# Performance work log

Hardware: AMD Instinct MI355X
Metric: run time of the kernel (lower is better)

## Reference

```python
import jax, jax.numpy as jnp
import numpy as np

EPS = 1e-5

def conv1x1(x, w, b):
    # x: (B,C,H,W), w: (O,C), b: (O,)
    return jnp.einsum('bchw,oc->bohw', x, w) + b[None, :, None, None]

def instance_norm(x):
    mu = jnp.mean(x, axis=(2, 3), keepdims=True)
    var = jnp.var(x, axis=(2, 3), keepdims=True)
    return (x - mu) / jnp.sqrt(var + EPS)

def setup_inputs() -> dict:
    key = jax.random.key(0)
    C = 256
    ks = jax.random.split(key, 16)
    def w(k):
        return jax.random.normal(k, (C, C), dtype=jnp.float32) * 0.02
    def b(k):
        return jax.random.normal(k, (C,), dtype=jnp.float32) * 0.01
    return {
        'x': jax.random.normal(ks[0], (8, C, 128, 128), dtype=jnp.float32),
        'wq1': w(ks[1]), 'bq1': b(ks[2]), 'wq2': w(ks[3]), 'bq2': b(ks[4]),
        'wk1': w(ks[5]), 'bk1': b(ks[6]), 'wk2': w(ks[7]), 'bk2': b(ks[8]),
        'wv': w(ks[9]), 'bv': b(ks[10]),
        'wg': w(ks[11]), 'bg': b(ks[12]),
        'wo': w(ks[13]), 'bo': b(ks[14]),
    }

def reference(x, wq1, bq1, wq2, bq2, wk1, bk1, wk2, bk2, wv, bv, wg, bg, wo, bo):
    head = 4
    B, C, H, W = x.shape
    c = C // head  # per-head channels
    n = H * W
    x = instance_norm(x)
    q = jax.nn.softplus(conv1x1(jax.nn.gelu(conv1x1(x, wq1, bq1), approximate=False), wq2, bq2))
    k = jax.nn.softplus(conv1x1(jax.nn.gelu(conv1x1(x, wk1, bk1), approximate=False), wk2, bk2))
    v = jax.nn.gelu(conv1x1(x, wv, bv), approximate=False)
    g = jax.nn.gelu(conv1x1(x, wg, bg), approximate=False)
    # b (head c) h w -> b head c (h w)
    q = q.reshape(B, head, c, n)
    kk = k.reshape(B, head, c, n)
    vv = v.reshape(B, head, c, n)
    kv = jnp.einsum('bhcn,bhdn->bhcd', kk, vv)  # (B,head,c,c)
    scale = 1.0 / jnp.sqrt(jnp.float32(c))
    z = jnp.einsum('bhcn,bhc->bhn', q, kk.sum(axis=-1)) * scale
    z = 1.0 / (z + jnp.float32(n))
    out = jnp.einsum('bhcn,bhcd->bhdn', q, kv) * scale
    out = (out + vv) * z[:, :, None, :]
    out = out.reshape(B, C, H, W)
    out = out * g
    return conv1x1(out, wo, bo)
```

## Files before the change

### kernel.cpp

```cpp
#include <hip/hip_runtime.h>
#include <stdint.h>

typedef short bf8 __attribute__((ext_vector_type(8)));
typedef short s4v __attribute__((ext_vector_type(4)));
typedef float f32x4 __attribute__((ext_vector_type(4)));

__device__ __forceinline__ short f2bf(float f){
  union { float f; unsigned u; } c; c.f = f;
  unsigned r = (c.u + 0x7fffu + ((c.u >> 16) & 1u)) >> 16;
  return (short)r;
}
__device__ __forceinline__ float bf2f(short s){
  union { unsigned u; float f; } c; c.u = ((unsigned)(unsigned short)s) << 16;
  return c.f;
}
__device__ __forceinline__ void gload16(const void* g, void* l){
  __builtin_amdgcn_global_load_lds((const __attribute__((address_space(1))) uint32_t*)g,
                                   (__attribute__((address_space(3))) uint32_t*)l, 16, 0, 0);
}
__device__ __forceinline__ float fast_erf(float x){
  const float s = fabsf(x);
  const float t = __builtin_amdgcn_rcpf(fmaf(0.3275911f, s, 1.0f));
  float p = fmaf(1.061405429f, t, -1.453152027f);
  p = fmaf(p, t, 1.421413741f);
  p = fmaf(p, t, -0.284496736f);
  p = fmaf(p, t, 0.254829592f);
  p = p * t;
  const float e = __expf(-s * s);
  return copysignf(fmaf(-p, e, 1.0f), x);
}
__device__ __forceinline__ float act_gelu(float x){
  return 0.5f * x * (1.0f + fast_erf(x * 0.70710678118654752f));
}
__device__ __forceinline__ float act_softplus(float x){
  const float e = __expf(-fabsf(x));
  return fmaxf(x, 0.0f) + __logf(1.0f + e);
}

__global__ __launch_bounds__(256) void k_statst(const float* __restrict__ x, short* __restrict__ xt,
                                                float* __restrict__ ps1, float* __restrict__ ps2){
  const int n0 = blockIdx.x * 64, c0 = blockIdx.y * 64, b = blockIdx.z;
  __shared__ short lt[64][68];
  const int t = threadIdx.x, nj = (t & 15) * 4, cb = t >> 4;
  float s1[4] = {0.f,0.f,0.f,0.f}, s2[4] = {0.f,0.f,0.f,0.f};
#pragma unroll
  for (int it = 0; it < 4; ++it){
    const int ci = cb + it * 16;
    const int row = b * 256 + c0 + ci;
    float4 v = *(const float4*)(x + (size_t)row * 16384 + n0 + nj);
    s4v o;
    o[0] = f2bf(v.x); o[1] = f2bf(v.y); o[2] = f2bf(v.z); o[3] = f2bf(v.w);
    *(s4v*)(&lt[ci][nj]) = o;
    s1[it] += v.x + v.y + v.z + v.w;
    s2[it] += v.x*v.x + v.y*v.y + v.z*v.z + v.w*v.w;
  }
  __syncthreads();
#pragma unroll
  for (int p = 0; p < 2; ++p){
    const int q = p * 256 + t;
    const int nl = q >> 3, c8 = (q & 7) * 8;
    bf8 o;
#pragma unroll
    for (int j = 0; j < 8; ++j) o[j] = lt[c8 + j][nl];
    *(bf8*)(xt + ((size_t)(b * 16384 + n0 + nl)) * 256 + c0 + c8) = o;
  }
#pragma unroll
  for (int it = 0; it < 4; ++it){
#pragma unroll
    for (int off = 8; off > 0; off >>= 1){
      s1[it] += __shfl_down(s1[it], off);
      s2[it] += __shfl_down(s2[it], off);
    }
  }
  if ((t & 15) == 0){
#pragma unroll
    for (int it = 0; it < 4; ++it){
      const int c = c0 + cb + it * 16;
      ps1[((size_t)(b * 256 + c)) * 256 + blockIdx.x] = s1[it];
      ps2[((size_t)(b * 256 + c)) * 256 + blockIdx.x] = s2[it];
    }
  }
}

__global__ __launch_bounds__(256) void k_red(const float* __restrict__ ps1, const float* __restrict__ ps2,
                                             float* __restrict__ mu, float* __restrict__ rsig){
  const int bc = blockIdx.x;
  const int t = threadIdx.x;
  __shared__ float a1[256], a2[256];
  a1[t] = ps1[(size_t)bc * 256 + t];
  a2[t] = ps2[(size_t)bc * 256 + t];
  __syncthreads();
  for (int s = 128; s > 0; s >>= 1){
    if (t < s){ a1[t] += a1[t+s]; a2[t] += a2[t+s]; }
    __syncthreads();
  }
  if (t == 0){
    float m = a1[0] * (1.0f/16384.0f);
    float v = a2[0] * (1.0f/16384.0f) - m*m;
    mu[bc] = m; rsig[bc] = rsqrtf(v + 1e-5f);
  }
}

__global__ __launch_bounds__(256) void k_norm(short* xn, const float* __restrict__ mu,
                                              const float* __restrict__ rsig){
  const int g = blockIdx.x * 256 + threadIdx.x;
#pragma unroll
  for (int pass = 0; pass < 8; ++pass){
    const int idx = g + pass * 524288;
    const int bn = idx >> 5, c8 = idx & 31;
    const int b = bn >> 14;
    const float* mp = mu + b * 256 + c8 * 8;
    const float* rp = rsig + b * 256 + c8 * 8;
    float4 m0 = *(const float4*)mp, m1 = *(const float4*)(mp + 4);
    float4 r0 = *(const float4*)rp, r1 = *(const float4*)(rp + 4);
    float mm[8] = {m0.x,m0.y,m0.z,m0.w,m1.x,m1.y,m1.z,m1.w};
    float rr[8] = {r0.x,r0.y,r0.z,r0.w,r1.x,r1.y,r1.z,r1.w};
    bf8 v = *(const bf8*)(xn + (size_t)idx * 8);
    bf8 o;
#pragma unroll
    for (int j = 0; j < 8; ++j) o[j] = f2bf((bf2f(v[j]) - mm[j]) * rr[j]);
    *(bf8*)(xn + (size_t)idx * 8) = o;
  }
}

__global__ __launch_bounds__(256) void k_wconv(const float* w0, const float* w1, const float* w2,
                                               const float* w3, const float* w4, const float* w5,
                                               const float* w6, short* __restrict__ wb){
  const int gid = blockIdx.x * 256 + threadIdx.x;
  const int mat = gid >> 14, r4 = gid & 16383;
  const float* srcs[7] = {w0, w1, w2, w3, w4, w5, w6};
  float4 v = *(const float4*)(srcs[mat] + (size_t)r4 * 4);
  s4v o; o[0] = f2bf(v.x); o[1] = f2bf(v.y); o[2] = f2bf(v.z); o[3] = f2bf(v.w);
  *(s4v*)(wb + (size_t)mat * 65536 + r4 * 4) = o;
}

template<int ACT>
__global__ __launch_bounds__(256, 2)
void k_gemm0(const short* __restrict__ A, const short* __restrict__ W,
             const float* __restrict__ bias, short* __restrict__ outp){
  __shared__ short sA[2][128 * 32];
  __shared__ short sB[2][256 * 32];
  const int t = threadIdx.x, l = t & 63, w = t >> 6;
  const int wr = w >> 1, wc = w & 1;
  const int lm = l & 15, lk = l >> 4;
  const size_t m0 = (size_t)blockIdx.x * 128;
  const int swz = ((lk ^ ((lm >> 1) & 3)) << 4);
  f32x4 acc[4][8] = {};

  auto stage = [&](int ks, int buf){
    const int k0 = ks * 32;
#pragma unroll
    for (int p = 0; p < 2; ++p){
      const int q = p * 256 + t, r = q >> 2, kc = q & 3;
      gload16(A + (m0 + r) * 256 + k0 + ((kc ^ ((r >> 1) & 3)) << 3),
              (char*)(&sA[buf][0]) + (p * 256 + w * 64) * 16);
    }
#pragma unroll
    for (int p = 0; p < 4; ++p){
      const int q = p * 256 + t, r = q >> 2, kc = q & 3;
      gload16(W + (size_t)r * 256 + k0 + ((kc ^ ((r >> 1) & 3)) << 3),
              (char*)(&sB[buf][0]) + (p * 256 + w * 64) * 16);
    }
  };

  stage(0, 0);
  __syncthreads();
  int cur = 0;
  for (int ks = 0; ks < 8; ++ks){
    if (ks < 7) stage(ks + 1, cur ^ 1);
    bf8 af[4], bfv[8];
#pragma unroll
    for (int mi = 0; mi < 4; ++mi)
      af[mi] = *(const bf8*)((const char*)(&sA[cur][0]) + (wr * 64 + mi * 16 + lm) * 64 + swz);
#pragma unroll
    for (int ni = 0; ni < 8; ++ni)
      bfv[ni] = *(const bf8*)((const char*)(&sB[cur][0]) + (wc * 128 + ni * 16 + lm) * 64 + swz);
#pragma unroll
    for (int mi = 0; mi < 4; ++mi)
#pragma unroll
      for (int ni = 0; ni < 8; ++ni)
        acc[mi][ni] = __builtin_amdgcn_mfma_f32_16x16x32_bf16(bfv[ni], af[mi], acc[mi][ni], 0, 0, 0);
    __syncthreads();
    cur ^= 1;
  }

#pragma unroll
  for (int ni = 0; ni < 8; ++ni){
    const int ob = wc * 128 + ni * 16 + lk * 4;
    const float4 b4 = *(const float4*)(bias + ob);
#pragma unroll
    for (int mi = 0; mi < 4; ++mi){
      const int px = wr * 64 + mi * 16 + lm;
      s4v o4;
#pragma unroll
      for (int j = 0; j < 4; ++j){
        float v = acc[mi][ni][j] + ((const float*)&b4)[j];
        if (ACT == 1) v = act_gelu(v);
        else if (ACT == 2) v = act_softplus(v);
        o4[j] = f2bf(v);
      }
      *(s4v*)(outp + (m0 + px) * 256 + ob) = o4;
    }
  }
}

__global__ __launch_bounds__(256, 2)
void k_chain(const short* __restrict__ A, const short* __restrict__ W1, const float* __restrict__ b1,
             const short* __restrict__ W2, const float* __restrict__ b2, short* __restrict__ out){
  __shared__ short sA[2][64 * 32];
  __shared__ short sB[2][256 * 32];
  __shared__ short h1[64 * 256];
  const int t = threadIdx.x, l = t & 63, w = t >> 6;
  const int lm = l & 15, lk = l >> 4;
  const size_t m0 = (size_t)blockIdx.x * 64;
  const int swz = ((lk ^ ((lm >> 1) & 3)) << 4);
  f32x4 acc[4][4] = {};

  auto stageA = [&](int ks, int buf){
    const int r = t >> 2, kc = t & 3;
    gload16(A + (m0 + r) * 256 + ks * 32 + ((kc ^ ((r >> 1) & 3)) << 3),
            (char*)(&sA[buf][0]) + w * 1024);
  };
  auto stageW = [&](const short* Wm, int ks, int buf){
#pragma unroll
    for (int p = 0; p < 4; ++p){
      const int q = p * 256 + t, r = q >> 2, kc = q & 3;
      gload16(Wm + (size_t)r * 256 + ks * 32 + ((kc ^ ((r >> 1) & 3)) << 3),
              (char*)(&sB[buf][0]) + (p * 256 + w * 64) * 16);
    }
  };

  stageA(0, 0); stageW(W1, 0, 0);
  __syncthreads();
  int cur = 0;
  for (int ks = 0; ks < 8; ++ks){
    if (ks < 7){ stageA(ks + 1, cur ^ 1); stageW(W1, ks + 1, cur ^ 1); }
    bf8 af[4], bfv[4];
#pragma unroll
    for (int mi = 0; mi < 4; ++mi)
      af[mi] = *(const bf8*)((const char*)(&sA[cur][0]) + (mi * 16 + lm) * 64 + swz);
#pragma unroll
    for (int ni = 0; ni < 4; ++ni)
      bfv[ni] = *(const bf8*)((const char*)(&sB[cur][0]) + (w * 64 + ni * 16 + lm) * 64 + swz);
#pragma unroll
    for (int mi = 0; mi < 4; ++mi)
#pragma unroll
      for (int ni = 0; ni < 4; ++ni)
        acc[mi][ni] = __builtin_amdgcn_mfma_f32_16x16x32_bf16(bfv[ni], af[mi], acc[mi][ni], 0, 0, 0);
    __syncthreads();
    cur ^= 1;
  }

  stageW(W2, 0, 0);
#pragma unroll
  for (int ni = 0; ni < 4; ++ni){
    const int ob = w * 64 + ni * 16 + lk * 4;
    const float4 b4 = *(const float4*)(b1 + ob);
#pragma unroll
    for (int mi = 0; mi < 4; ++mi){
      const int px = mi * 16 + lm;
      s4v o4;
#pragma unroll
      for (int j = 0; j < 4; ++j)
        o4[j] = f2bf(act_gelu(acc[mi][ni][j] + ((const float*)&b4)[j]));
      const int slot = (ob >> 3) ^ (px & 7);
      *(s4v*)((char*)h1 + px * 512 + (slot << 4) + (ob & 4) * 2) = o4;
      acc[mi][ni] = (f32x4){0.f, 0.f, 0.f, 0.f};
    }
  }
  __syncthreads();

  cur = 0;
  for (int ks = 0; ks < 8; ++ks){
    if (ks < 7) stageW(W2, ks + 1, cur ^ 1);
    bf8 af[4], bfv[4];
#pragma unroll
    for (int mi = 0; mi < 4; ++mi){
      const int row = mi * 16 + lm;
      const int slot = (ks * 4 + lk) ^ (row & 7);
      af[mi] = *(const bf8*)((const char*)h1 + row * 512 + (slot << 4));
    }
#pragma unroll
    for (int ni = 0; ni < 4; ++ni)
      bfv[ni] = *(const bf8*)((const char*)(&sB[cur][0]) + (w * 64 + ni * 16 + lm) * 64 + swz);
#pragma unroll
    for (int mi = 0; mi < 4; ++mi)
#pragma unroll
      for (int ni = 0; ni < 4; ++ni)
        acc[mi][ni] = __builtin_amdgcn_mfma_f32_16x16x32_bf16(bfv[ni], af[mi], acc[mi][ni], 0, 0, 0);
    __syncthreads();
    cur ^= 1;
  }
#pragma unroll
  for (int ni = 0; ni < 4; ++ni){
    const int ob = w * 64 + ni * 16 + lk * 4;
    const float4 b4 = *(const float4*)(b2 + ob);
#pragma unroll
    for (int mi = 0; mi < 4; ++mi){
      const int px = mi * 16 + lm;
      s4v o4;
#pragma unroll
      for (int j = 0; j < 4; ++j)
        o4[j] = f2bf(act_softplus(acc[mi][ni][j] + ((const float*)&b4)[j]));
      *(s4v*)(out + (m0 + px) * 256 + ob) = o4;
    }
  }
}

__global__ __launch_bounds__(256) void k_kv(const short* __restrict__ kg, const short* __restrict__ vg,
                                            float* __restrict__ kvpart, float* __restrict__ kspart){
  const int s = blockIdx.x, h = blockIdx.y, b = blockIdx.z;
  __shared__ short sk[64 * 72], sv[64 * 72];
  __shared__ float pl[256][8];
  const int t = threadIdx.x, l = t & 63, w = t >> 6;
  const int lm = l & 15, lk = l >> 4;
  float ksp[8];
#pragma unroll
  for (int j = 0; j < 8; ++j) ksp[j] = 0.f;
  f32x4 acc[4] = {};
  const size_t rowbase = ((size_t)b * 16384 + s * 2048) * 256 + h * 64;

  for (int tt = 0; tt < 32; ++tt){
    __syncthreads();
#pragma unroll
    for (int p = 0; p < 2; ++p){
      const int q = p * 256 + t;
      const int nl = q >> 3, c8 = (q & 7) * 8;
      bf8 kvv = *(const bf8*)(kg + rowbase + (size_t)(tt * 64 + nl) * 256 + c8);
      bf8 vvv = *(const bf8*)(vg + rowbase + (size_t)(tt * 64 + nl) * 256 + c8);
#pragma unroll
      for (int j = 0; j < 8; ++j){
        sk[(c8 + j) * 72 + nl] = kvv[j];
        sv[(c8 + j) * 72 + nl] = vvv[j];
        ksp[j] += bf2f(kvv[j]);
      }
    }
    __syncthreads();
#pragma unroll
    for (int ks = 0; ks < 2; ++ks){
      bf8 ak = *(const bf8*)((const char*)sk + (w * 16 + lm) * 144 + ks * 64 + lk * 16);
#pragma unroll
      for (int ni = 0; ni < 4; ++ni){
        bf8 bv = *(const bf8*)((const char*)sv + (ni * 16 + lm) * 144 + ks * 64 + lk * 16);
        acc[ni] = __builtin_amdgcn_mfma_f32_16x16x32_bf16(ak, bv, acc[ni], 0, 0, 0);
      }
    }
  }
#pragma unroll
  for (int j = 0; j < 8; ++j) pl[t][j] = ksp[j];
  __syncthreads();
  const size_t slot = (size_t)(b * 4 + h) * 8 + s;
  if (t < 64){
    float sum = 0.f;
    const int g8 = t >> 3, j = t & 7;
    for (int m = 0; m < 32; ++m) sum += pl[m * 8 + g8][j];
    kspart[slot * 64 + t] = sum;
  }
  float* kvp = kvpart + slot * 4096;
#pragma unroll
  for (int ni = 0; ni < 4; ++ni)
#pragma unroll
    for (int j = 0; j < 4; ++j){
      const int c = w * 16 + lk * 4 + j, d = ni * 16 + lm;
      kvp[c * 64 + d] = acc[ni][j];
    }
}

__global__ __launch_bounds__(256) void k_kvred(const float* __restrict__ kvpart, const float* __restrict__ kspart,
                                               short* __restrict__ kvT, float* __restrict__ ksum_s){
  const int gid = blockIdx.x * 256 + threadIdx.x;
#pragma unroll
  for (int i = 0; i < 8; ++i){
    const int o = gid * 8 + i;
    const int bh = o >> 12, rem = o & 4095, d = rem >> 6, c = rem & 63;
    float sum = 0.f;
#pragma unroll
    for (int s = 0; s < 8; ++s) sum += kvpart[((size_t)bh * 8 + s) * 4096 + c * 64 + d];
    kvT[o] = f2bf(sum * 0.125f);
  }
  if (gid < 2048){
    float sum = 0.f;
#pragma unroll
    for (int s = 0; s < 8; ++s) sum += kspart[((size_t)(gid >> 6) * 8 + s) * 64 + (gid & 63)];
    ksum_s[gid] = sum * 0.125f;
  }
}

__global__ __launch_bounds__(256, 2)
void k_fuse(const short* __restrict__ xn, const short* __restrict__ qg,
            const short* __restrict__ vg, const short* __restrict__ kvT,
            const float* __restrict__ ksum_s,
            const short* __restrict__ Wg, const float* __restrict__ bg,
            const short* __restrict__ Wo, const float* __restrict__ bo,
            float* __restrict__ outp){
  __shared__ short sA[2][64 * 32];
  __shared__ short sB[2][256 * 32];
  __shared__ short yl[64 * 256];
  __shared__ float sz[256];
  __shared__ float sks[256];
  const int t = threadIdx.x, l = t & 63, w = t >> 6;
  const int lm = l & 15, lk = l >> 4;
  const size_t m0 = (size_t)blockIdx.x * 64;
  const int b = (int)(m0 >> 14);
  const int h = w;
  const int swz = ((lk ^ ((lm >> 1) & 3)) << 4);

  sks[t] = ksum_s[b * 256 + t];

  auto stageA = [&](int ks, int buf){
    const int r = t >> 2, kc = t & 3;
    gload16(xn + (m0 + r) * 256 + ks * 32 + ((kc ^ ((r >> 1) & 3)) << 3),
            (char*)(&sA[buf][0]) + w * 1024);
  };
  auto stageW = [&](const short* Wm, int ks, int buf){
#pragma unroll
    for (int p = 0; p < 4; ++p){
      const int q = p * 256 + t, r = q >> 2, kc = q & 3;
      gload16(Wm + (size_t)r * 256 + ks * 32 + ((kc ^ ((r >> 1) & 3)) << 3),
              (char*)(&sB[buf][0]) + (p * 256 + w * 64) * 16);
    }
  };

  f32x4 acc[4][4] = {};

  stageA(0, 0); stageW(Wg, 0, 0);
  __syncthreads();
  int cur = 0;
  for (int ks = 0; ks < 8; ++ks){
    if (ks < 7){ stageA(ks + 1, cur ^ 1); stageW(Wg, ks + 1, cur ^ 1); }
    bf8 af[4], bfv[4];
#pragma unroll
    for (int mi = 0; mi < 4; ++mi)
      af[mi] = *(const bf8*)((const char*)(&sA[cur][0]) + (mi * 16 + lm) * 64 + swz);
#pragma unroll
    for (int ni = 0; ni < 4; ++ni)
      bfv[ni] = *(const bf8*)((const char*)(&sB[cur][0]) + (w * 64 + ni * 16 + lm) * 64 + swz);
#pragma unroll
    for (int mi = 0; mi < 4; ++mi)
#pragma unroll
      for (int ni = 0; ni < 4; ++ni)
        acc[mi][ni] = __builtin_amdgcn_mfma_f32_16x16x32_bf16(bfv[ni], af[mi], acc[mi][ni], 0, 0, 0);
    __syncthreads();
    cur ^= 1;
  }
  s4v g_pk[4][4];
#pragma unroll
  for (int ni = 0; ni < 4; ++ni){
    const int ob = h * 64 + ni * 16 + lk * 4;
    const float4 b4 = *(const float4*)(bg + ob);
#pragma unroll
    for (int mi = 0; mi < 4; ++mi){
#pragma unroll
      for (int j = 0; j < 4; ++j)
        g_pk[mi][ni][j] = f2bf(act_gelu(acc[mi][ni][j] + ((const float*)&b4)[j]));
      acc[mi][ni] = (f32x4){0.f, 0.f, 0.f, 0.f};
    }
  }

  {
    float dot = 0.f;
#pragma unroll
    for (int cc = 0; cc < 8; ++cc){
      bf8 qv = *(const bf8*)(qg + (m0 + l) * 256 + h * 64 + cc * 8);
#pragma unroll
      for (int j = 0; j < 8; ++j) dot += bf2f(qv[j]) * sks[h * 64 + cc * 8 + j];
    }
    sz[h * 64 + l] = 1.0f / (dot + 16384.0f);
  }

  const short* kvb = kvT + (size_t)b * 16384;
#pragma unroll
  for (int ks = 0; ks < 2; ++ks){
    bf8 aq[4];
#pragma unroll
    for (int mi = 0; mi < 4; ++mi)
      aq[mi] = *(const bf8*)(qg + (m0 + mi * 16 + lm) * 256 + h * 64 + ks * 32 + lk * 8);
#pragma unroll
    for (int ni = 0; ni < 4; ++ni){
      bf8 bk = *(const bf8*)(kvb + (size_t)(h * 64 + ni * 16 + lm) * 64 + ks * 32 + lk * 8);
#pragma unroll
      for (int mi = 0; mi < 4; ++mi)
        acc[mi][ni] = __builtin_amdgcn_mfma_f32_16x16x32_bf16(bk, aq[mi], acc[mi][ni], 0, 0, 0);
    }
  }
#pragma unroll
  for (int mi = 0; mi < 4; ++mi){
    const int px = mi * 16 + lm;
    const float zf = sz[h * 64 + px];
    const size_t base = (m0 + px) * 256;
#pragma unroll
    for (int ni = 0; ni < 4; ++ni){
      const int ch = h * 64 + ni * 16 + lk * 4;
      s4v v4 = *(const s4v*)(vg + base + ch);
      s4v o4;
#pragma unroll
      for (int j = 0; j < 4; ++j)
        o4[j] = f2bf((acc[mi][ni][j] + bf2f(v4[j])) * zf * bf2f(g_pk[mi][ni][j]));
      const int slot = (ch >> 3) ^ (px & 7);
      *(s4v*)((char*)yl + px * 512 + (slot << 4) + (ch & 4) * 2) = o4;
      acc[mi][ni] = (f32x4){0.f, 0.f, 0.f, 0.f};
    }
  }
  stageW(Wo, 0, 0);
  __syncthreads();

  cur = 0;
  for (int ks = 0; ks < 8; ++ks){
    if (ks < 7) stageW(Wo, ks + 1, cur ^ 1);
    bf8 af[4], bfv[4];
#pragma unroll
    for (int mi = 0; mi < 4; ++mi){
      const int row = mi * 16 + lm;
      const int slot = (ks * 4 + lk) ^ (row & 7);
      af[mi] = *(const bf8*)((const char*)yl + row * 512 + (slot << 4));
    }
#pragma unroll
    for (int ni = 0; ni < 4; ++ni)
      bfv[ni] = *(const bf8*)((const char*)(&sB[cur][0]) + (w * 64 + ni * 16 + lm) * 64 + swz);
#pragma unroll
    for (int mi = 0; mi < 4; ++mi)
#pragma unroll
      for (int ni = 0; ni < 4; ++ni)
        acc[mi][ni] = __builtin_amdgcn_mfma_f32_16x16x32_bf16(af[mi], bfv[ni], acc[mi][ni], 0, 0, 0);
    __syncthreads();
    cur ^= 1;
  }
  const int nb = (int)(m0 & 16383);
#pragma unroll
  for (int mi = 0; mi < 4; ++mi){
    const int np = nb + mi * 16 + lk * 4;
#pragma unroll
    for (int ni = 0; ni < 4; ++ni){
      const int o = w * 64 + ni * 16 + lm;
      const float bi = bo[o];
      float4 v;
      v.x = acc[mi][ni][0] + bi; v.y = acc[mi][ni][1] + bi;
      v.z = acc[mi][ni][2] + bi; v.w = acc[mi][ni][3] + bi;
      *(float4*)(outp + (((size_t)(b * 256 + o)) * 16384 + np)) = v;
    }
  }
}

extern "C" void kernel_launch(void* const* d_in, const int* in_sizes, int n_in,
                              void* d_out, int out_size, void* d_ws, size_t ws_size,
                              hipStream_t stream){
  (void)in_sizes; (void)n_in; (void)out_size; (void)ws_size;
  const float* x   = (const float*)d_in[0];
  const float* wq1 = (const float*)d_in[1];
  const float* bq1 = (const float*)d_in[2];
  const float* wq2 = (const float*)d_in[3];
  const float* bq2 = (const float*)d_in[4];
  const float* wk1 = (const float*)d_in[5];
  const float* bk1 = (const float*)d_in[6];
  const float* wk2 = (const float*)d_in[7];
  const float* bk2 = (const float*)d_in[8];
  const float* wv  = (const float*)d_in[9];
  const float* bv  = (const float*)d_in[10];
  const float* wg  = (const float*)d_in[11];
  const float* bg  = (const float*)d_in[12];
  const float* wo  = (const float*)d_in[13];
  const float* bo  = (const float*)d_in[14];

  char* ws = (char*)d_ws;
  float* mu     = (float*)(ws + 0);
  float* rsig   = (float*)(ws + 8192);
  short* wb     = (short*)(ws + 16384);
  float* kvpart = (float*)(ws + 933888);
  float* ps1    = (float*)(ws + 933888);
  float* ps2    = (float*)(ws + 3031040);
  float* kspart = (float*)(ws + 5128192);
  short* kvT    = (short*)(ws + 5193728);
  float* ksum_s = (float*)(ws + 5455872);
  short* B0 = (short*)(ws + 8388608);
  short* B1 = B0 + 33554432;
  short* B2 = B1 + 33554432;
  short* B3 = B2 + 33554432;

  k_wconv<<<448, 256, 0, stream>>>(wq1, wq2, wk1, wk2, wv, wg, wo, wb);
  k_statst<<<dim3(256, 4, 8), 256, 0, stream>>>(x, B0, ps1, ps2);
  k_red<<<2048, 256, 0, stream>>>(ps1, ps2, mu, rsig);
  k_norm<<<2048, 256, 0, stream>>>(B0, mu, rsig);
  k_chain<<<2048, 256, 0, stream>>>(B0, wb + 0 * 65536, bq1, wb + 1 * 65536, bq2, B2);
  k_chain<<<2048, 256, 0, stream>>>(B0, wb + 2 * 65536, bk1, wb + 3 * 65536, bk2, B3);
  k_gemm0<1><<<1024, 256, 0, stream>>>(B0, wb + 4 * 65536, bv, B1);
  k_kv<<<dim3(8, 4, 8), 256, 0, stream>>>(B3, B1, kvpart, kspart);
  k_kvred<<<64, 256, 0, stream>>>(kvpart, kspart, kvT, ksum_s);
  k_fuse<<<2048, 256, 0, stream>>>(B0, B2, B1, kvT, ksum_s,
                                   wb + 5 * 65536, bg, wb + 6 * 65536, bo,
                                   (float*)d_out);
}
```

Measured before the change: 446.0 us.

## Fold instance-norm into per-batch first-layer weights and biases, drop normalize pass

Removes the separate normalization kernel. The per-channel mean and inverse std are folded into batch-specific bf16 copies of the four first-layer weight matrices, with adjusted biases, built by a new small kernel. The GEMM kernels index those copies by batch, and only the remaining weights are converted to bf16. The k/v reduction grid is also halved to four sequence slices per head, each doing twice the work. This saves a full read-modify-write pass over the activations, but the GEMMs now consume raw unnormalized bf16 inputs, which may change precision, and the kv kernel runs with fewer blocks.

Result: slower. 525.7 us (+17.9%).

```diff
diff --git a/kernel.cpp b/kernel.cpp
--- a/kernel.cpp
+++ b/kernel.cpp
@@ -101,34 +101,44 @@
   }
 }
 
-__global__ __launch_bounds__(256) void k_norm(short* xn, const float* __restrict__ mu,
-                                              const float* __restrict__ rsig){
-  const int g = blockIdx.x * 256 + threadIdx.x;
-#pragma unroll
-  for (int pass = 0; pass < 8; ++pass){
-    const int idx = g + pass * 524288;
-    const int bn = idx >> 5, c8 = idx & 31;
-    const int b = bn >> 14;
-    const float* mp = mu + b * 256 + c8 * 8;
-    const float* rp = rsig + b * 256 + c8 * 8;
-    float4 m0 = *(const float4*)mp, m1 = *(const float4*)(mp + 4);
-    float4 r0 = *(const float4*)rp, r1 = *(const float4*)(rp + 4);
-    float mm[8] = {m0.x,m0.y,m0.z,m0.w,m1.x,m1.y,m1.z,m1.w};
-    float rr[8] = {r0.x,r0.y,r0.z,r0.w,r1.x,r1.y,r1.z,r1.w};
-    bf8 v = *(const bf8*)(xn + (size_t)idx * 8);
-    bf8 o;
-#pragma unroll
-    for (int j = 0; j < 8; ++j) o[j] = f2bf((bf2f(v[j]) - mm[j]) * rr[j]);
-    *(bf8*)(xn + (size_t)idx * 8) = o;
+__global__ __launch_bounds__(256) void k_wfold(
+    const float* __restrict__ w0, const float* __restrict__ bb0,
+    const float* __restrict__ w1, const float* __restrict__ bb1,
+    const float* __restrict__ w2, const float* __restrict__ bb2,
+    const float* __restrict__ w3, const float* __restrict__ bb3,
+    const float* __restrict__ mu, const float* __restrict__ rsig,
+    short* __restrict__ wf, float* __restrict__ bf){
+  const int m = blockIdx.x >> 3, b = blockIdx.x & 7;
+  const float* Wm = (m==0)?w0:(m==1)?w1:(m==2)?w2:w3;
+  const float* Bm = (m==0)?bb0:(m==1)?bb1:(m==2)?bb2:bb3;
+  __shared__ float rs[256], ms[256];
+  const int t = threadIdx.x;
+  rs[t] = rsig[b*256+t];
+  ms[t] = mu[b*256+t] * rs[t];
+  __syncthreads();
+  short* wout = wf + ((size_t)(m*8+b)) * 65536;
+  float* bout = bf + (m*8+b) * 256;
+  const int lane = t & 63, wv = t >> 6;
+  for (int oi = 0; oi < 64; ++oi){
+    const int o = oi * 4 + wv;
+    const int c = lane * 4;
+    float4 w4 = *(const float4*)(Wm + (size_t)o * 256 + c);
+    float pa = w4.x*ms[c] + w4.y*ms[c+1] + w4.z*ms[c+2] + w4.w*ms[c+3];
+    s4v o4;
+    o4[0] = f2bf(w4.x*rs[c]);   o4[1] = f2bf(w4.y*rs[c+1]);
+    o4[2] = f2bf(w4.z*rs[c+2]); o4[3] = f2bf(w4.w*rs[c+3]);
+    *(s4v*)(wout + (size_t)o * 256 + c) = o4;
+#pragma unroll
+    for (int off = 32; off > 0; off >>= 1) pa += __shfl_down(pa, off);
+    if (lane == 0) bout[o] = Bm[o] - pa;
   }
 }
 
 __global__ __launch_bounds__(256) void k_wconv(const float* w0, const float* w1, const float* w2,
-                                               const float* w3, const float* w4, const float* w5,
-                                               const float* w6, short* __restrict__ wb){
+                                               short* __restrict__ wb){
   const int gid = blockIdx.x * 256 + threadIdx.x;
   const int mat = gid >> 14, r4 = gid & 16383;
-  const float* srcs[7] = {w0, w1, w2, w3, w4, w5, w6};
+  const float* srcs[3] = {w0, w1, w2};
   float4 v = *(const float4*)(srcs[mat] + (size_t)r4 * 4);
   s4v o; o[0] = f2bf(v.x); o[1] = f2bf(v.y); o[2] = f2bf(v.z); o[3] = f2bf(v.w);
   *(s4v*)(wb + (size_t)mat * 65536 + r4 * 4) = o;
@@ -136,14 +146,17 @@
 
 template<int ACT>
 __global__ __launch_bounds__(256, 2)
-void k_gemm0(const short* __restrict__ A, const short* __restrict__ W,
-             const float* __restrict__ bias, short* __restrict__ outp){
+void k_gemm0(const short* __restrict__ A, const short* __restrict__ Wf,
+             const float* __restrict__ bfold, short* __restrict__ outp){
   __shared__ short sA[2][128 * 32];
   __shared__ short sB[2][256 * 32];
   const int t = threadIdx.x, l = t & 63, w = t >> 6;
   const int wr = w >> 1, wc = w & 1;
   const int lm = l & 15, lk = l >> 4;
   const size_t m0 = (size_t)blockIdx.x * 128;
+  const int b = (int)(m0 >> 14);
+  const short* W = Wf + (size_t)b * 65536;
+  const float* bias = bfold + b * 256;
   const int swz = ((lk ^ ((lm >> 1) & 3)) << 4);
   f32x4 acc[4][8] = {};
 
@@ -205,7 +218,7 @@
 }
 
 __global__ __launch_bounds__(256, 2)
-void k_chain(const short* __restrict__ A, const short* __restrict__ W1, const float* __restrict__ b1,
+void k_chain(const short* __restrict__ A, const short* __restrict__ W1f, const float* __restrict__ b1f,
              const short* __restrict__ W2, const float* __restrict__ b2, short* __restrict__ out){
   __shared__ short sA[2][64 * 32];
   __shared__ short sB[2][256 * 32];
@@ -213,6 +226,9 @@
   const int t = threadIdx.x, l = t & 63, w = t >> 6;
   const int lm = l & 15, lk = l >> 4;
   const size_t m0 = (size_t)blockIdx.x * 64;
+  const int b = (int)(m0 >> 14);
+  const short* W1 = W1f + (size_t)b * 65536;
+  const float* b1 = b1f + b * 256;
   const int swz = ((lk ^ ((lm >> 1) & 3)) << 4);
   f32x4 acc[4][4] = {};
 
@@ -318,9 +334,9 @@
 #pragma unroll
   for (int j = 0; j < 8; ++j) ksp[j] = 0.f;
   f32x4 acc[4] = {};
-  const size_t rowbase = ((size_t)b * 16384 + s * 2048) * 256 + h * 64;
-
-  for (int tt = 0; tt < 32; ++tt){
+  const size_t rowbase = ((size_t)b * 16384 + s * 4096) * 256 + h * 64;
+
+  for (int tt = 0; tt < 64; ++tt){
     __syncthreads();
 #pragma unroll
     for (int p = 0; p < 2; ++p){
@@ -349,7 +365,7 @@
 #pragma unroll
   for (int j = 0; j < 8; ++j) pl[t][j] = ksp[j];
   __syncthreads();
-  const size_t slot = (size_t)(b * 4 + h) * 8 + s;
+  const size_t slot = (size_t)(b * 4 + h) * 4 + s;
   if (t < 64){
     float sum = 0.f;
     const int g8 = t >> 3, j = t & 7;
@@ -375,22 +391,22 @@
     const int bh = o >> 12, rem = o & 4095, d = rem >> 6, c = rem & 63;
     float sum = 0.f;
 #pragma unroll
-    for (int s = 0; s < 8; ++s) sum += kvpart[((size_t)bh * 8 + s) * 4096 + c * 64 + d];
+    for (int s = 0; s < 4; ++s) sum += kvpart[((size_t)bh * 4 + s) * 4096 + c * 64 + d];
     kvT[o] = f2bf(sum * 0.125f);
   }
   if (gid < 2048){
     float sum = 0.f;
 #pragma unroll
-    for (int s = 0; s < 8; ++s) sum += kspart[((size_t)(gid >> 6) * 8 + s) * 64 + (gid & 63)];
+    for (int s = 0; s < 4; ++s) sum += kspart[((size_t)(gid >> 6) * 4 + s) * 64 + (gid & 63)];
     ksum_s[gid] = sum * 0.125f;
   }
 }
 
 __global__ __launch_bounds__(256, 2)
-void k_fuse(const short* __restrict__ xn, const short* __restrict__ qg,
+void k_fuse(const short* __restrict__ xt, const short* __restrict__ qg,
             const short* __restrict__ vg, const short* __restrict__ kvT,
             const float* __restrict__ ksum_s,
-            const short* __restrict__ Wg, const float* __restrict__ bg,
+            const short* __restrict__ Wgf, const float* __restrict__ bgf,
             const short* __restrict__ Wo, const float* __restrict__ bo,
             float* __restrict__ outp){
   __shared__ short sA[2][64 * 32];
@@ -403,13 +419,15 @@
   const size_t m0 = (size_t)blockIdx.x * 64;
   const int b = (int)(m0 >> 14);
   const int h = w;
+  const short* Wg = Wgf + (size_t)b * 65536;
+  const float* bg = bgf + b * 256;
   const int swz = ((lk ^ ((lm >> 1) & 3)) << 4);
 
   sks[t] = ksum_s[b * 256 + t];
 
   auto stageA = [&](int ks, int buf){
     const int r = t >> 2, kc = t & 3;
-    gload16(xn + (m0 + r) * 256 + ks * 32 + ((kc ^ ((r >> 1) & 3)) << 3),
+    gload16(xt + (m0 + r) * 256 + ks * 32 + ((kc ^ ((r >> 1) & 3)) << 3),
             (char*)(&sA[buf][0]) + w * 1024);
   };
   auto stageW = [&](const short* Wm, int ks, int buf){
@@ -565,27 +583,31 @@
   float* mu     = (float*)(ws + 0);
   float* rsig   = (float*)(ws + 8192);
   short* wb     = (short*)(ws + 16384);
-  float* kvpart = (float*)(ws + 933888);
-  float* ps1    = (float*)(ws + 933888);
-  float* ps2    = (float*)(ws + 3031040);
-  float* kspart = (float*)(ws + 5128192);
-  short* kvT    = (short*)(ws + 5193728);
-  float* ksum_s = (float*)(ws + 5455872);
+  float* bfold  = (float*)(ws + 409600);
+  short* wf     = (short*)(ws + 442368);
+  float* ps1    = (float*)(ws + 442368);
+  float* ps2    = (float*)(ws + 2539520);
+  float* kvpart = (float*)(ws + 4636672);
+  float* kspart = (float*)(ws + 6733824);
+  short* kvT    = (short*)(ws + 6766592);
+  float* ksum_s = (float*)(ws + 7028736);
   short* B0 = (short*)(ws + 8388608);
   short* B1 = B0 + 33554432;
   short* B2 = B1 + 33554432;
   short* B3 = B2 + 33554432;
 
-  k_wconv<<<448, 256, 0, stream>>>(wq1, wq2, wk1, wk2, wv, wg, wo, wb);
+  k_wconv<<<192, 256, 0, stream>>>(wq2, wk2, wo, wb);
   k_statst<<<dim3(256, 4, 8), 256, 0, stream>>>(x, B0, ps1, ps2);
   k_red<<<2048, 256, 0, stream>>>(ps1, ps2, mu, rsig);
-  k_norm<<<2048, 256, 0, stream>>>(B0, mu, rsig);
-  k_chain<<<2048, 256, 0, stream>>>(B0, wb + 0 * 65536, bq1, wb + 1 * 65536, bq2, B2);
-  k_chain<<<2048, 256, 0, stream>>>(B0, wb + 2 * 65536, bk1, wb + 3 * 65536, bk2, B3);
-  k_gemm0<1><<<1024, 256, 0, stream>>>(B0, wb + 4 * 65536, bv, B1);
-  k_kv<<<dim3(8, 4, 8), 256, 0, stream>>>(B3, B1, kvpart, kspart);
+  k_wfold<<<32, 256, 0, stream>>>(wq1, bq1, wk1, bk1, wv, bv, wg, bg, mu, rsig, wf, bfold);
+  k_chain<<<2048, 256, 0, stream>>>(B0, wf + 0 * 524288, bfold + 0 * 2048,
+                                    wb + 0 * 65536, bq2, B2);
+  k_chain<<<2048, 256, 0, stream>>>(B0, wf + 1 * 524288, bfold + 1 * 2048,
+                                    wb + 1 * 65536, bk2, B3);
+  k_gemm0<1><<<1024, 256, 0, stream>>>(B0, wf + 2 * 524288, bfold + 2 * 2048, B1);
+  k_kv<<<dim3(4, 4, 8), 256, 0, stream>>>(B3, B1, kvpart, kspart);
   k_kvred<<<64, 256, 0, stream>>>(kvpart, kspart, kvT, ksum_s);
   k_fuse<<<2048, 256, 0, stream>>>(B0, B2, B1, kvT, ksum_s,
-                                   wb + 5 * 65536, bg, wb + 6 * 65536, bo,
-                                   (float*)d_out);
-}
+                                   wf + 3 * 524288, bfold + 3 * 2048,
+                                   wb + 2 * 65536, bo, (float*)d_out);
+}
```

## Prefetch two stages ahead with explicit vmcnt waits and raw barriers

Applied to the files above, without the earlier changes.

The GEMM main loops in several kernels now issue the global-to-LDS loads for two k-steps before the loop starts. Each iteration waits with a partial s_waitcnt vmcnt until only the newest stage is still outstanding, then refills the buffer it just consumed with stage ks+2 after a raw s_barrier. This replaces the full __syncthreads drains, so global loads overlap more with MFMA work. The hand-counted vmcnt values must match the number of loads each stage issues, and any mismatch would cause data races.

New measurement: 442.1 us. No clear change (-0.9%).

```diff
diff --git a/kernel.cpp b/kernel.cpp
--- a/kernel.cpp
+++ b/kernel.cpp
@@ -4,6 +4,11 @@
 typedef short bf8 __attribute__((ext_vector_type(8)));
 typedef short s4v __attribute__((ext_vector_type(4)));
 typedef float f32x4 __attribute__((ext_vector_type(4)));
+
+#define VM_WAIT(N) asm volatile("s_waitcnt vmcnt(" #N ")" ::: "memory")
+#define LGKM0()    asm volatile("s_waitcnt lgkmcnt(0)" ::: "memory")
+#define SBAR()     do { __builtin_amdgcn_sched_barrier(0); __builtin_amdgcn_s_barrier(); \
+                        __builtin_amdgcn_sched_barrier(0); } while (0)
 
 __device__ __forceinline__ short f2bf(float f){
   union { float f; unsigned u; } c; c.f = f;
@@ -164,10 +169,11 @@
   };
 
   stage(0, 0);
-  __syncthreads();
-  int cur = 0;
+  stage(1, 1);
   for (int ks = 0; ks < 8; ++ks){
-    if (ks < 7) stage(ks + 1, cur ^ 1);
+    const int cur = ks & 1;
+    if (ks < 7) { VM_WAIT(6); } else { VM_WAIT(0); }
+    SBAR();
     bf8 af[4], bfv[8];
 #pragma unroll
     for (int mi = 0; mi < 4; ++mi)
@@ -180,8 +186,8 @@
 #pragma unroll
       for (int ni = 0; ni < 8; ++ni)
         acc[mi][ni] = __builtin_amdgcn_mfma_f32_16x16x32_bf16(bfv[ni], af[mi], acc[mi][ni], 0, 0, 0);
-    __syncthreads();
-    cur ^= 1;
+    SBAR();
+    if (ks < 6) stage(ks + 2, cur);
   }
 
 #pragma unroll
@@ -231,10 +237,11 @@
   };
 
   stageA(0, 0); stageW(W1, 0, 0);
-  __syncthreads();
-  int cur = 0;
+  stageA(1, 1); stageW(W1, 1, 1);
   for (int ks = 0; ks < 8; ++ks){
-    if (ks < 7){ stageA(ks + 1, cur ^ 1); stageW(W1, ks + 1, cur ^ 1); }
+    const int cur = ks & 1;
+    if (ks < 7) { VM_WAIT(5); } else { VM_WAIT(0); }
+    SBAR();
     bf8 af[4], bfv[4];
 #pragma unroll
     for (int mi = 0; mi < 4; ++mi)
@@ -247,11 +254,10 @@
 #pragma unroll
       for (int ni = 0; ni < 4; ++ni)
         acc[mi][ni] = __builtin_amdgcn_mfma_f32_16x16x32_bf16(bfv[ni], af[mi], acc[mi][ni], 0, 0, 0);
-    __syncthreads();
-    cur ^= 1;
-  }
-
-  stageW(W2, 0, 0);
+    SBAR();
+    if (ks < 6){ stageA(ks + 2, cur); stageW(W1, ks + 2, cur); }
+  }
+
 #pragma unroll
   for (int ni = 0; ni < 4; ++ni){
     const int ob = w * 64 + ni * 16 + lk * 4;
@@ -268,11 +274,13 @@
       acc[mi][ni] = (f32x4){0.f, 0.f, 0.f, 0.f};
     }
   }
-  __syncthreads();
-
-  cur = 0;
+  stageW(W2, 0, 0); stageW(W2, 1, 1);
+  LGKM0();
+
   for (int ks = 0; ks < 8; ++ks){
-    if (ks < 7) stageW(W2, ks + 1, cur ^ 1);
+    const int cur = ks & 1;
+    if (ks < 7) { VM_WAIT(4); } else { VM_WAIT(0); }
+    SBAR();
     bf8 af[4], bfv[4];
 #pragma unroll
     for (int mi = 0; mi < 4; ++mi){
@@ -288,8 +296,8 @@
 #pragma unroll
       for (int ni = 0; ni < 4; ++ni)
         acc[mi][ni] = __builtin_amdgcn_mfma_f32_16x16x32_bf16(bfv[ni], af[mi], acc[mi][ni], 0, 0, 0);
-    __syncthreads();
-    cur ^= 1;
+    SBAR();
+    if (ks < 6) stageW(W2, ks + 2, cur);
   }
 #pragma unroll
   for (int ni = 0; ni < 4; ++ni){
@@ -424,10 +432,11 @@
   f32x4 acc[4][4] = {};
 
   stageA(0, 0); stageW(Wg, 0, 0);
-  __syncthreads();
-  int cur = 0;
+  stageA(1, 1); stageW(Wg, 1, 1);
   for (int ks = 0; ks < 8; ++ks){
-    if (ks < 7){ stageA(ks + 1, cur ^ 1); stageW(Wg, ks + 1, cur ^ 1); }
+    const int cur = ks & 1;
+    if (ks < 7) { VM_WAIT(5); } else { VM_WAIT(0); }
+    SBAR();
     bf8 af[4], bfv[4];
 #pragma unroll
     for (int mi = 0; mi < 4; ++mi)
@@ -440,8 +449,8 @@
 #pragma unroll
       for (int ni = 0; ni < 4; ++ni)
         acc[mi][ni] = __builtin_amdgcn_mfma_f32_16x16x32_bf16(bfv[ni], af[mi], acc[mi][ni], 0, 0, 0);
-    __syncthreads();
-    cur ^= 1;
+    SBAR();
+    if (ks < 6){ stageA(ks + 2, cur); stageW(Wg, ks + 2, cur); }
   }
   s4v g_pk[4][4];
 #pragma unroll
@@ -501,12 +510,13 @@
       acc[mi][ni] = (f32x4){0.f, 0.f, 0.f, 0.f};
     }
   }
-  stageW(Wo, 0, 0);
-  __syncthreads();
-
-  cur = 0;
+  stageW(Wo, 0, 0); stageW(Wo, 1, 1);
+  LGKM0();
+
   for (int ks = 0; ks < 8; ++ks){
-    if (ks < 7) stageW(Wo, ks + 1, cur ^ 1);
+    const int cur = ks & 1;
+    if (ks < 7) { VM_WAIT(4); } else { VM_WAIT(0); }
+    SBAR();
     bf8 af[4], bfv[4];
 #pragma unroll
     for (int mi = 0; mi < 4; ++mi){
@@ -522,8 +532,8 @@
 #pragma unroll
       for (int ni = 0; ni < 4; ++ni)
         acc[mi][ni] = __builtin_amdgcn_mfma_f32_16x16x32_bf16(af[mi], bfv[ni], acc[mi][ni], 0, 0, 0);
-    __syncthreads();
-    cur ^= 1;
+    SBAR();
+    if (ks < 6) stageW(Wo, ks + 2, cur);
   }
   const int nb = (int)(m0 & 16383);
 #pragma unroll
```
